# Optimization experiments

Hardware: AMD Instinct MI355X
Metric: run time of the kernel (lower is better)

## Reference

```python
import jax, jax.numpy as jnp
import numpy as np

D_MODEL = 640
KW = 32                                  # kernel_width -> content_kernel (compression (1,1))
SUPER = np.array([5, 5, 2, 1, 1])        # supersampling per subhead
DIL = np.array([1, 1, 2, 4, 8])          # dilation rate per subhead
SUBHEADS = 5
HEADS = int(SUPER.sum())                 # 14
DH = D_MODEL // SUBHEADS                 # 128
B, N = 2, 1024
KC = KW                                  # content kernel width
DIL_PER_HEAD = np.repeat(DIL, SUPER)     # dilation used by each of the 14 value heads


def _windows(seq, bias, dil):
    """Banded (dilated, stride-1, 'same'-padded) windows of a projected sequence.

    seq: (B, N, DH). The original zero-pads the raw sequence, then applies the
    per-head Linear; projecting a zero vector yields the bias, so padding the
    projected sequence with `bias` is mathematically identical.
    Returns (B, N, KC, DH) with out[b, l, j] = padded[b, l + j*dil].
    """
    dil = int(dil)
    pad_total = (KC - 1) * dil           # effective kernel minus 1, stride 1 -> same length
    pl = pad_total // 2
    pr = pad_total - pl
    b = seq.shape[0]
    left = jnp.broadcast_to(bias, (b, pl, DH))
    right = jnp.broadcast_to(bias, (b, pr, DH))
    padded = jnp.concatenate([left, seq, right], axis=1)
    idx = jnp.arange(N)[:, None] + jnp.arange(KC)[None, :] * dil  # (N, KC)
    return padded[:, idx]


def setup_inputs() -> dict:
    key = jax.random.key(0)
    ks = jax.random.split(key, 13)
    f = lambda k, sh, s=1.0: jax.random.normal(k, sh, dtype=jnp.float32) * s
    return {
        "query": f(ks[0], (B, N, D_MODEL)),
        "key": f(ks[1], (B, N, D_MODEL)),
        "value": f(ks[2], (B, N, D_MODEL)),
        "Qk": f(ks[3], (SUBHEADS, DH, D_MODEL), 0.04),
        "Qb": f(ks[4], (SUBHEADS, DH), 0.02),
        "Kk": f(ks[5], (SUBHEADS, DH, D_MODEL), 0.04),
        "Kb": f(ks[6], (SUBHEADS, DH), 0.02),
        "Vk": f(ks[7], (HEADS, DH, D_MODEL), 0.04),
        "Vb": f(ks[8], (HEADS, DH), 0.02),
        "Sk": f(ks[9], (HEADS, KC, KC), 0.1),   # Pos_Sampling kernel, Kq=1 so in=out=KC
        "Sb": f(ks[10], (HEADS, KC), 0.02),
        "Ck": f(ks[11], (D_MODEL, HEADS * DH), 0.02),  # Collapse kernel
        "Cb": f(ks[12], (D_MODEL,), 0.0),
    }


def reference(query, key, value, Qk, Qb, Kk, Kb, Vk, Vb, Sk, Sb, Ck, Cb):
    # Per-subhead Q/K projections (query_kernel=1, stride=1 -> one query per position)
    q = jnp.einsum('bnd,sod->bnso', query, Qk) + Qb          # (B,N,5,DH)
    kproj = jnp.einsum('bnd,sod->bnso', key, Kk) + Kb        # (B,N,5,DH)
    kwin = jnp.stack(
        [_windows(kproj[:, :, s], Kb[s], DIL[s]) for s in range(SUBHEADS)],
        axis=2)                                              # (B,N,5,KC,DH)
    # Banded scores (original applies no 1/sqrt(d) scaling)
    score = jnp.einsum('bnsd,bnskd->bnsk', q, kwin)          # (B,N,5,KC)
    # Supersample subhead scores into heads, then learned positional resampling
    score = jnp.repeat(score, SUPER, axis=2, total_repeat_length=HEADS)  # (B,N,14,KC)
    score = jnp.einsum('bnhk,hjk->bnhj', score, Sk) + Sb     # Pos_Sampling Linear
    w = jax.nn.softmax(score, axis=-1)
    # Per-head value projection; each head windows with its subhead's dilation
    vproj = jnp.einsum('bnd,hod->bnho', value, Vk) + Vb      # (B,N,14,DH)
    vwin = jnp.stack(
        [_windows(vproj[:, :, h], Vb[h], DIL_PER_HEAD[h]) for h in range(HEADS)],
        axis=2)                                              # (B,N,14,KC,DH)
    attn = jnp.einsum('bnhk,bnhkd->bnhd', w, vwin)           # (B,N,14,DH)
    flat = attn.reshape(attn.shape[0], attn.shape[1], HEADS * DH)
    return jnp.einsum('bnf,of->bno', flat, Ck) + Cb          # (B,N,D_MODEL)
```

## Files before the change

kernel.cpp:

```cpp
#include <hip/hip_runtime.h>
#include <hip/hip_bf16.h>

using bf16 = __hip_bfloat16;
typedef __attribute__((ext_vector_type(8))) short s16x8;
typedef __attribute__((ext_vector_type(4))) float f32x4;
typedef unsigned int u32;

__device__ __forceinline__ float b2f(short u) {
    union { float f; u32 i; } x; x.i = ((u32)(unsigned short)u) << 16; return x.f;
}
__device__ __forceinline__ short f2b(float f) {
    bf16 h = (bf16)f; return *(short*)&h;
}

__device__ __forceinline__ void glds16(const bf16* g, bf16* l) {
#if __has_builtin(__builtin_amdgcn_global_load_lds)
    __builtin_amdgcn_global_load_lds(
        (const __attribute__((address_space(1))) u32*)g,
        (__attribute__((address_space(3))) u32*)l, 16, 0, 0);
#else
    *(uint4*)l = *(const uint4*)g;
#endif
}

__global__ void sniff_kernel(const u32* __restrict__ probe, int* __restrict__ flag) {
    __shared__ int bad;
    if (threadIdx.x == 0) bad = 0;
    __syncthreads();
    int myb = 0;
    for (int i = threadIdx.x; i < 512; i += 256) {
        u32 e = (probe[i] >> 7) & 0xFFu;
        if (e >= 0xF0u) myb = 1;
    }
    if (myb) atomicOr(&bad, 1);
    __syncthreads();
    if (threadIdx.x == 0) *flag = bad ? 1 : 0;
}

struct CvtArgs {
    const void* src[13];
    bf16* dst[13];
    int n[13];
    int bb[14];
};
__global__ __launch_bounds__(256)
void convert_kernel(CvtArgs a, const int* __restrict__ flagp) {
    const int f32 = *flagp;
    const int blk = blockIdx.x;
    int s = 0;
    while (s < 12 && blk >= a.bb[s + 1]) ++s;
    const int base = (blk - a.bb[s]) * 1024 + threadIdx.x * 4;
    if (base >= a.n[s]) return;
    bf16* dst = a.dst[s] + base;
    if (f32) {
        float4 v = *((const float4*)a.src[s] + (base >> 2));
        dst[0] = (bf16)v.x; dst[1] = (bf16)v.y; dst[2] = (bf16)v.z; dst[3] = (bf16)v.w;
    } else {
        *(ushort4*)dst = *((const ushort4*)a.src[s] + (base >> 2));
    }
}

template<int BM, int BN, int OUT>
__global__ __launch_bounds__(256)
void gemm_v2(const bf16* __restrict__ A0, const bf16* __restrict__ W0,
             const bf16* __restrict__ b0, void* __restrict__ o0,
             const bf16* __restrict__ A1, const bf16* __restrict__ W1,
             const bf16* __restrict__ b1, void* __restrict__ o1,
             int M, int N, int K, const int* __restrict__ flagp) {
    const bf16* A    = blockIdx.z ? A1 : A0;
    const bf16* W    = blockIdx.z ? W1 : W0;
    const bf16* bias = blockIdx.z ? b1 : b0;
    void*       out  = blockIdx.z ? o1 : o0;
    constexpr int WM = BM / 2, WN = BN / 2, FM = WM / 16, FN = WN / 16;
    constexpr int SA = (BM * 4) / 256, SB = (BN * 4) / 256;
    __shared__ __align__(16) bf16 lA[BM * 32];
    __shared__ __align__(16) bf16 lB[BN * 32];
    const int tid = threadIdx.x;
    const int wave = tid >> 6, lane = tid & 63;
    const int wr = wave >> 1, wc = wave & 1;
    const int quad = lane >> 4, lm = lane & 15;
    const int m0 = blockIdx.x * BM, n0 = blockIdx.y * BN;
    f32x4 acc[FM][FN] = {};
    for (int k0 = 0; k0 < K; k0 += 32) {
#pragma unroll
        for (int q = 0; q < SA; ++q) {
            int sl = q * 256 + tid;
            glds16(A + (size_t)(m0 + (sl >> 2)) * K + k0 + (sl & 3) * 8, lA + sl * 8);
        }
#pragma unroll
        for (int q = 0; q < SB; ++q) {
            int sl = q * 256 + tid;
            glds16(W + (size_t)(n0 + (sl >> 2)) * K + k0 + (sl & 3) * 8, lB + sl * 8);
        }
        __syncthreads();
        s16x8 afr[FM], bfr[FN];
#pragma unroll
        for (int i = 0; i < FM; ++i)
            afr[i] = *(const s16x8*)&lA[(wr * WM + i * 16 + lm) * 32 + quad * 8];
#pragma unroll
        for (int j = 0; j < FN; ++j)
            bfr[j] = *(const s16x8*)&lB[(wc * WN + j * 16 + lm) * 32 + quad * 8];
#pragma unroll
        for (int i = 0; i < FM; ++i)
#pragma unroll
            for (int j = 0; j < FN; ++j)
                acc[i][j] = __builtin_amdgcn_mfma_f32_16x16x32_bf16(afr[i], bfr[j], acc[i][j], 0, 0, 0);
        __syncthreads();
    }
    const int f32out = (OUT == 0) ? 1 : (OUT == 1) ? 0 : *flagp;
#pragma unroll
    for (int i = 0; i < FM; ++i) {
        const int rbase = m0 + wr * WM + i * 16 + quad * 4;
#pragma unroll
        for (int j = 0; j < FN; ++j) {
            const int col = n0 + wc * WN + j * 16 + lm;
            const float bv = (float)bias[col];
#pragma unroll
            for (int r = 0; r < 4; ++r) {
                float v = acc[i][j][r] + bv;
                size_t off = (size_t)(rbase + r) * N + col;
                if (f32out) ((float*)out)[off] = v;
                else        ((bf16*)out)[off] = (bf16)v;
            }
        }
    }
}

__global__ __launch_bounds__(256)
void attn_v2(const float* __restrict__ qp, const float* __restrict__ kp,
             const bf16* __restrict__ vp,
             const bf16* __restrict__ Kbc, const bf16* __restrict__ Vbc,
             const bf16* __restrict__ Skc, const bf16* __restrict__ Sbc,
             bf16* __restrict__ atn) {
    const int pos = blockIdx.x, b = pos >> 10, l = pos & 1023;
    const int t = threadIdx.x;
    __shared__ float qs[640];
    __shared__ float partA[5 * 256];
    __shared__ float sc5[5 * 32];
    __shared__ float sc14[14 * 32];
    __shared__ float w14[14 * 32];

    for (int i = t; i < 640; i += 256) qs[i] = qp[(size_t)pos * 640 + i];
    __syncthreads();

    {
        const int j = t >> 3, part = t & 7, cbase = part * 16;
#pragma unroll
        for (int s = 0; s < 5; ++s) {
            const int dil = (s < 2) ? 1 : (1 << (s - 1));
            const int pl = (31 * dil) >> 1;
            const int row = l + j * dil - pl;
            const float* q = qs + s * 128 + cbase;
            float acc = 0.f;
            if (row >= 0 && row < 1024) {
                const float* kr = kp + (size_t)((b << 10) | row) * 640 + s * 128 + cbase;
#pragma unroll
                for (int c = 0; c < 16; c += 4) {
                    float4 kv = *(const float4*)(kr + c);
                    acc += q[c] * kv.x + q[c + 1] * kv.y + q[c + 2] * kv.z + q[c + 3] * kv.w;
                }
            } else {
                const bf16* kb = Kbc + s * 128 + cbase;
#pragma unroll
                for (int c = 0; c < 16; ++c) acc += q[c] * (float)kb[c];
            }
            partA[s * 256 + t] = acc;
        }
    }
    __syncthreads();
    if (t < 160) {
        const int s = t >> 5, j = t & 31;
        const float* p = partA + s * 256 + j * 8;
        sc5[s * 32 + j] = ((p[0] + p[1]) + (p[2] + p[3])) + ((p[4] + p[5]) + (p[6] + p[7]));
    }
    __syncthreads();

    {
        int idx = t;
#pragma unroll
        for (int rep = 0; rep < 2; ++rep, idx += 256) {
            if (idx < 448) {
                const int h = idx >> 5;
                const int s = (h < 5) ? 0 : (h < 10) ? 1 : (h < 12) ? 2 : (h == 12) ? 3 : 4;
                float acc = b2f(((const short*)Sbc)[idx]);
                const short* sk = (const short*)Skc + idx * 32;
                const float* sc = sc5 + s * 32;
#pragma unroll
                for (int k = 0; k < 32; ++k) acc += sc[k] * b2f(sk[k]);
                sc14[idx] = acc;
            }
        }
    }
    __syncthreads();

    if (t < 14) {
        const float* srow = sc14 + t * 32;
        float* wrow = w14 + t * 32;
        float mx = srow[0];
        for (int j = 1; j < 32; ++j) mx = fmaxf(mx, srow[j]);
        float sum = 0.f;
        for (int j = 0; j < 32; ++j) { float e = __expf(srow[j] - mx); wrow[j] = e; sum += e; }
        float inv = 1.f / sum;
        for (int j = 0; j < 32; ++j) wrow[j] *= inv;
    }
    __syncthreads();

    if (t < 224) {
        const int h = t >> 4, d8 = (t & 15) * 8;
        const int dil = (h < 10) ? 1 : (h < 12) ? 2 : (h == 12) ? 4 : 8;
        const int pl = (31 * dil) >> 1;
        const int col = h * 128 + d8;
        const float* wrow = w14 + h * 32;
        float acc[8] = {};
#pragma unroll
        for (int j = 0; j < 32; ++j) {
            const int row = l + j * dil - pl;
            const short* src = (row >= 0 && row < 1024)
                ? (const short*)vp + (size_t)((b << 10) | row) * 1792 + col
                : (const short*)Vbc + col;
            s16x8 v8 = *(const s16x8*)src;
            const float w = wrow[j];
#pragma unroll
            for (int r = 0; r < 8; ++r) acc[r] += w * b2f(v8[r]);
        }
        union { uint4 u; short h16[8]; } o;
#pragma unroll
        for (int r = 0; r < 8; ++r) o.h16[r] = f2b(acc[r]);
        *(uint4*)((short*)atn + (size_t)pos * 1792 + col) = o.u;
    }
}

extern "C" void kernel_launch(void* const* d_in, const int* in_sizes, int n_in,
                              void* d_out, int out_size, void* d_ws, size_t ws_size,
                              hipStream_t stream) {
    const int M = 2048;
    char* w = (char*)d_ws;
    size_t off = 0;
    auto alloc = [&](size_t bytes) -> char* {
        off = (off + 255) & ~(size_t)255;
        char* p = w + off; off += bytes; return p;
    };
    int*  flagp = (int*)alloc(4);
    bf16* qc  = (bf16*)alloc((size_t)M * 640 * 2);
    bf16* kc  = (bf16*)alloc((size_t)M * 640 * 2);
    bf16* vc  = (bf16*)alloc((size_t)M * 640 * 2);
    bf16* Qkc = (bf16*)alloc(409600 * 2);
    bf16* Kkc = (bf16*)alloc(409600 * 2);
    bf16* Vkc = (bf16*)alloc(1146880 * 2);
    bf16* Ckc = (bf16*)alloc(1146880 * 2);
    bf16* Qbc = (bf16*)alloc(640 * 2);
    bf16* Kbc = (bf16*)alloc(640 * 2);
    bf16* Vbc = (bf16*)alloc(1792 * 2);
    bf16* Skc = (bf16*)alloc(14336 * 2);
    bf16* Sbc = (bf16*)alloc(448 * 2);
    bf16* Cbc = (bf16*)alloc(640 * 2);
    float* qp = (float*)alloc((size_t)M * 640 * 4);
    float* kp = (float*)alloc((size_t)M * 640 * 4);
    bf16*  vp = (bf16*)alloc((size_t)M * 1792 * 2);
    bf16*  atn = qc;

    dim3 blk(256);
    sniff_kernel<<<dim3(1), blk, 0, stream>>>((const u32*)d_in[3], flagp);

    CvtArgs ca;
    const int srcIdx[13] = {0, 1, 2, 3, 4, 5, 6, 7, 8, 9, 10, 11, 12};
    bf16* dsts[13] = {qc, kc, vc, Qkc, Qbc, Kkc, Kbc, Vkc, Vbc, Skc, Sbc, Ckc, Cbc};
    const int ns[13] = {1310720, 1310720, 1310720, 409600, 640, 409600, 640,
                        1146880, 1792, 14336, 448, 1146880, 640};
    int cum = 0;
    for (int i = 0; i < 13; ++i) {
        ca.src[i] = d_in[srcIdx[i]];
        ca.dst[i] = dsts[i];
        ca.n[i] = ns[i];
        ca.bb[i] = cum;
        cum += (ns[i] + 1023) / 1024;
    }
    ca.bb[13] = cum;
    convert_kernel<<<dim3(cum), blk, 0, stream>>>(ca, flagp);

    gemm_v2<64, 64, 0><<<dim3(32, 10, 2), blk, 0, stream>>>(
        qc, Qkc, Qbc, qp, kc, Kkc, Kbc, kp, M, 640, 640, flagp);
    gemm_v2<64, 64, 1><<<dim3(32, 28, 1), blk, 0, stream>>>(
        vc, Vkc, Vbc, vp, vc, Vkc, Vbc, vp, M, 1792, 640, flagp);
    attn_v2<<<dim3(2048), blk, 0, stream>>>(qp, kp, vp, Kbc, Vbc, Skc, Sbc, atn);
    gemm_v2<64, 64, 2><<<dim3(32, 10, 1), blk, 0, stream>>>(
        atn, Ckc, Cbc, d_out, atn, Ckc, Cbc, d_out, M, 640, 1792, flagp);
}
```

Measured before the change: 183.1 us.

## Fuse QKV projections into one kernel and drop the dtype sniff and activation conversion

Removes the dtype-sniff kernel and the runtime flag, assuming fp32 inputs. The activations are no longer converted to bf16 in a separate pass; the projection GEMM reads fp32 directly and converts while staging into LDS. The Q, K and V projections are merged into one launch, and block indices are remapped in the GEMM and attention kernels to group work by XCD for L2 locality. This cuts launches and a full read/write of the activations. The cost is that the A tile is now loaded synchronously instead of through the global-to-LDS load path.

```diff
diff --git a/kernel.cpp b/kernel.cpp
--- a/kernel.cpp
+++ b/kernel.cpp
@@ -23,116 +23,119 @@
 #endif
 }
 
-__global__ void sniff_kernel(const u32* __restrict__ probe, int* __restrict__ flag) {
-    __shared__ int bad;
-    if (threadIdx.x == 0) bad = 0;
-    __syncthreads();
-    int myb = 0;
-    for (int i = threadIdx.x; i < 512; i += 256) {
-        u32 e = (probe[i] >> 7) & 0xFFu;
-        if (e >= 0xF0u) myb = 1;
-    }
-    if (myb) atomicOr(&bad, 1);
-    __syncthreads();
-    if (threadIdx.x == 0) *flag = bad ? 1 : 0;
-}
-
-struct CvtArgs {
-    const void* src[13];
-    bf16* dst[13];
-    int n[13];
-    int bb[14];
-};
-__global__ __launch_bounds__(256)
-void convert_kernel(CvtArgs a, const int* __restrict__ flagp) {
-    const int f32 = *flagp;
+struct CvtArgs { const float* src[10]; bf16* dst[10]; int n[10]; int bb[11]; };
+__global__ __launch_bounds__(256)
+void convert_kernel(CvtArgs a) {
     const int blk = blockIdx.x;
     int s = 0;
-    while (s < 12 && blk >= a.bb[s + 1]) ++s;
+    while (s < 9 && blk >= a.bb[s + 1]) ++s;
     const int base = (blk - a.bb[s]) * 1024 + threadIdx.x * 4;
     if (base >= a.n[s]) return;
-    bf16* dst = a.dst[s] + base;
-    if (f32) {
-        float4 v = *((const float4*)a.src[s] + (base >> 2));
-        dst[0] = (bf16)v.x; dst[1] = (bf16)v.y; dst[2] = (bf16)v.z; dst[3] = (bf16)v.w;
-    } else {
-        *(ushort4*)dst = *((const ushort4*)a.src[s] + (base >> 2));
-    }
-}
-
-template<int BM, int BN, int OUT>
-__global__ __launch_bounds__(256)
-void gemm_v2(const bf16* __restrict__ A0, const bf16* __restrict__ W0,
-             const bf16* __restrict__ b0, void* __restrict__ o0,
-             const bf16* __restrict__ A1, const bf16* __restrict__ W1,
-             const bf16* __restrict__ b1, void* __restrict__ o1,
-             int M, int N, int K, const int* __restrict__ flagp) {
-    const bf16* A    = blockIdx.z ? A1 : A0;
-    const bf16* W    = blockIdx.z ? W1 : W0;
-    const bf16* bias = blockIdx.z ? b1 : b0;
-    void*       out  = blockIdx.z ? o1 : o0;
-    constexpr int WM = BM / 2, WN = BN / 2, FM = WM / 16, FN = WN / 16;
-    constexpr int SA = (BM * 4) / 256, SB = (BN * 4) / 256;
-    __shared__ __align__(16) bf16 lA[BM * 32];
-    __shared__ __align__(16) bf16 lB[BN * 32];
+    float4 v = *(const float4*)(a.src[s] + base);
+    ushort4 o;
+    o.x = (unsigned short)f2b(v.x); o.y = (unsigned short)f2b(v.y);
+    o.z = (unsigned short)f2b(v.z); o.w = (unsigned short)f2b(v.w);
+    *(ushort4*)(a.dst[s] + base) = o;
+}
+
+template<bool A_F32, bool OUT_F32>
+__device__ __forceinline__ void gemm64(
+    const void* __restrict__ A, const bf16* __restrict__ W,
+    const bf16* __restrict__ bias, void* __restrict__ out,
+    int m0, int n0, int N, int K, bf16* lA, bf16* lB) {
     const int tid = threadIdx.x;
     const int wave = tid >> 6, lane = tid & 63;
     const int wr = wave >> 1, wc = wave & 1;
     const int quad = lane >> 4, lm = lane & 15;
-    const int m0 = blockIdx.x * BM, n0 = blockIdx.y * BN;
-    f32x4 acc[FM][FN] = {};
+    const int srow = tid >> 2, scol8 = (tid & 3) * 8;
+    f32x4 acc[2][2] = {};
     for (int k0 = 0; k0 < K; k0 += 32) {
-#pragma unroll
-        for (int q = 0; q < SA; ++q) {
-            int sl = q * 256 + tid;
-            glds16(A + (size_t)(m0 + (sl >> 2)) * K + k0 + (sl & 3) * 8, lA + sl * 8);
-        }
-#pragma unroll
-        for (int q = 0; q < SB; ++q) {
-            int sl = q * 256 + tid;
-            glds16(W + (size_t)(n0 + (sl >> 2)) * K + k0 + (sl & 3) * 8, lB + sl * 8);
-        }
+        if (A_F32) {
+            const float* g = (const float*)A + (size_t)(m0 + srow) * K + k0 + scol8;
+            float4 f0 = *(const float4*)g;
+            float4 f1 = *(const float4*)(g + 4);
+            union { uint4 u; short h[8]; } p;
+            p.h[0] = f2b(f0.x); p.h[1] = f2b(f0.y); p.h[2] = f2b(f0.z); p.h[3] = f2b(f0.w);
+            p.h[4] = f2b(f1.x); p.h[5] = f2b(f1.y); p.h[6] = f2b(f1.z); p.h[7] = f2b(f1.w);
+            *(uint4*)(lA + tid * 8) = p.u;
+        } else {
+            glds16((const bf16*)A + (size_t)(m0 + srow) * K + k0 + scol8, lA + tid * 8);
+        }
+        glds16(W + (size_t)(n0 + srow) * K + k0 + scol8, lB + tid * 8);
         __syncthreads();
-        s16x8 afr[FM], bfr[FN];
-#pragma unroll
-        for (int i = 0; i < FM; ++i)
-            afr[i] = *(const s16x8*)&lA[(wr * WM + i * 16 + lm) * 32 + quad * 8];
-#pragma unroll
-        for (int j = 0; j < FN; ++j)
-            bfr[j] = *(const s16x8*)&lB[(wc * WN + j * 16 + lm) * 32 + quad * 8];
-#pragma unroll
-        for (int i = 0; i < FM; ++i)
-#pragma unroll
-            for (int j = 0; j < FN; ++j)
-                acc[i][j] = __builtin_amdgcn_mfma_f32_16x16x32_bf16(afr[i], bfr[j], acc[i][j], 0, 0, 0);
+        s16x8 af[2], bf[2];
+#pragma unroll
+        for (int i = 0; i < 2; ++i)
+            af[i] = *(const s16x8*)&lA[(wr * 32 + i * 16 + lm) * 32 + quad * 8];
+#pragma unroll
+        for (int j = 0; j < 2; ++j)
+            bf[j] = *(const s16x8*)&lB[(wc * 32 + j * 16 + lm) * 32 + quad * 8];
+#pragma unroll
+        for (int i = 0; i < 2; ++i)
+#pragma unroll
+            for (int j = 0; j < 2; ++j)
+                acc[i][j] = __builtin_amdgcn_mfma_f32_16x16x32_bf16(af[i], bf[j], acc[i][j], 0, 0, 0);
         __syncthreads();
     }
-    const int f32out = (OUT == 0) ? 1 : (OUT == 1) ? 0 : *flagp;
-#pragma unroll
-    for (int i = 0; i < FM; ++i) {
-        const int rbase = m0 + wr * WM + i * 16 + quad * 4;
-#pragma unroll
-        for (int j = 0; j < FN; ++j) {
-            const int col = n0 + wc * WN + j * 16 + lm;
+#pragma unroll
+    for (int i = 0; i < 2; ++i) {
+        const int rbase = m0 + wr * 32 + i * 16 + quad * 4;
+#pragma unroll
+        for (int j = 0; j < 2; ++j) {
+            const int col = n0 + wc * 32 + j * 16 + lm;
             const float bv = (float)bias[col];
 #pragma unroll
             for (int r = 0; r < 4; ++r) {
                 float v = acc[i][j][r] + bv;
                 size_t off = (size_t)(rbase + r) * N + col;
-                if (f32out) ((float*)out)[off] = v;
-                else        ((bf16*)out)[off] = (bf16)v;
+                if (OUT_F32) ((float*)out)[off] = v;
+                else         ((bf16*)out)[off] = (bf16)v;
             }
         }
     }
 }
 
 __global__ __launch_bounds__(256)
-void attn_v2(const float* __restrict__ qp, const float* __restrict__ kp,
+void proj_kernel(const float* __restrict__ q, const float* __restrict__ k,
+                 const float* __restrict__ v,
+                 const bf16* __restrict__ Qkc, const bf16* __restrict__ Kkc,
+                 const bf16* __restrict__ Vkc,
+                 const bf16* __restrict__ Qbc, const bf16* __restrict__ Kbc,
+                 const bf16* __restrict__ Vbc,
+                 float* __restrict__ qp, float* __restrict__ kp,
+                 bf16* __restrict__ vp) {
+    __shared__ __align__(16) bf16 lA[64 * 32];
+    __shared__ __align__(16) bf16 lB[64 * 32];
+    const int L = blockIdx.x, xcd = L & 7, i = L >> 3;
+    const int m0 = (xcd * 4 + i / 48) * 64;
+    const int nid = i % 48;
+    if (nid < 10)
+        gemm64<true, true >(q, Qkc, Qbc, qp, m0, nid * 64, 640, 640, lA, lB);
+    else if (nid < 20)
+        gemm64<true, true >(k, Kkc, Kbc, kp, m0, (nid - 10) * 64, 640, 640, lA, lB);
+    else
+        gemm64<true, false>(v, Vkc, Vbc, vp, m0, (nid - 20) * 64, 1792, 640, lA, lB);
+}
+
+__global__ __launch_bounds__(256)
+void collapse_kernel(const bf16* __restrict__ atn, const bf16* __restrict__ Ckc,
+                     const bf16* __restrict__ Cbc, float* __restrict__ out) {
+    __shared__ __align__(16) bf16 lA[64 * 32];
+    __shared__ __align__(16) bf16 lB[64 * 32];
+    const int L = blockIdx.x, xcd = L & 7, i = L >> 3;
+    const int m0 = (xcd * 4 + i / 10) * 64;
+    const int n0 = (i % 10) * 64;
+    gemm64<false, true>(atn, Ckc, Cbc, out, m0, n0, 640, 1792, lA, lB);
+}
+
+__global__ __launch_bounds__(256)
+void attn_v3(const float* __restrict__ qp, const float* __restrict__ kp,
              const bf16* __restrict__ vp,
              const bf16* __restrict__ Kbc, const bf16* __restrict__ Vbc,
              const bf16* __restrict__ Skc, const bf16* __restrict__ Sbc,
              bf16* __restrict__ atn) {
-    const int pos = blockIdx.x, b = pos >> 10, l = pos & 1023;
+    const int pos = ((blockIdx.x & 7) << 8) | (blockIdx.x >> 3);
+    const int b = pos >> 10, l = pos & 1023;
     const int t = threadIdx.x;
     __shared__ float qs[640];
     __shared__ float partA[5 * 256];
@@ -144,7 +147,7 @@
     __syncthreads();
 
     {
-        const int j = t >> 3, part = t & 7, cbase = part * 16;
+        const int j = t >> 3, cbase = (t & 7) * 16;
 #pragma unroll
         for (int s = 0; s < 5; ++s) {
             const int dil = (s < 2) ? 1 : (1 << (s - 1));
@@ -175,21 +178,19 @@
     }
     __syncthreads();
 
-    {
-        int idx = t;
-#pragma unroll
-        for (int rep = 0; rep < 2; ++rep, idx += 256) {
-            if (idx < 448) {
-                const int h = idx >> 5;
-                const int s = (h < 5) ? 0 : (h < 10) ? 1 : (h < 12) ? 2 : (h == 12) ? 3 : 4;
-                float acc = b2f(((const short*)Sbc)[idx]);
-                const short* sk = (const short*)Skc + idx * 32;
-                const float* sc = sc5 + s * 32;
-#pragma unroll
-                for (int k = 0; k < 32; ++k) acc += sc[k] * b2f(sk[k]);
-                sc14[idx] = acc;
-            }
-        }
+    for (int idx = t; idx < 448; idx += 256) {
+        const int h = idx >> 5;
+        const int s = (h < 5) ? 0 : (h < 10) ? 1 : (h < 12) ? 2 : (h == 12) ? 3 : 4;
+        const s16x8* sk = (const s16x8*)((const short*)Skc + idx * 32);
+        const float* sc = sc5 + s * 32;
+        float acc = b2f(((const short*)Sbc)[idx]);
+#pragma unroll
+        for (int g = 0; g < 4; ++g) {
+            s16x8 kk = sk[g];
+#pragma unroll
+            for (int r = 0; r < 8; ++r) acc += sc[g * 8 + r] * b2f(kk[r]);
+        }
+        sc14[idx] = acc;
     }
     __syncthreads();
 
@@ -240,49 +241,39 @@
         off = (off + 255) & ~(size_t)255;
         char* p = w + off; off += bytes; return p;
     };
-    int*  flagp = (int*)alloc(4);
-    bf16* qc  = (bf16*)alloc((size_t)M * 640 * 2);
-    bf16* kc  = (bf16*)alloc((size_t)M * 640 * 2);
-    bf16* vc  = (bf16*)alloc((size_t)M * 640 * 2);
     bf16* Qkc = (bf16*)alloc(409600 * 2);
+    bf16* Qbc = (bf16*)alloc(640 * 2);
     bf16* Kkc = (bf16*)alloc(409600 * 2);
+    bf16* Kbc = (bf16*)alloc(640 * 2);
     bf16* Vkc = (bf16*)alloc(1146880 * 2);
-    bf16* Ckc = (bf16*)alloc(1146880 * 2);
-    bf16* Qbc = (bf16*)alloc(640 * 2);
-    bf16* Kbc = (bf16*)alloc(640 * 2);
     bf16* Vbc = (bf16*)alloc(1792 * 2);
     bf16* Skc = (bf16*)alloc(14336 * 2);
     bf16* Sbc = (bf16*)alloc(448 * 2);
+    bf16* Ckc = (bf16*)alloc(1146880 * 2);
     bf16* Cbc = (bf16*)alloc(640 * 2);
     float* qp = (float*)alloc((size_t)M * 640 * 4);
     float* kp = (float*)alloc((size_t)M * 640 * 4);
     bf16*  vp = (bf16*)alloc((size_t)M * 1792 * 2);
-    bf16*  atn = qc;
-
-    dim3 blk(256);
-    sniff_kernel<<<dim3(1), blk, 0, stream>>>((const u32*)d_in[3], flagp);
+    bf16*  atn = (bf16*)alloc((size_t)M * 1792 * 2);
 
     CvtArgs ca;
-    const int srcIdx[13] = {0, 1, 2, 3, 4, 5, 6, 7, 8, 9, 10, 11, 12};
-    bf16* dsts[13] = {qc, kc, vc, Qkc, Qbc, Kkc, Kbc, Vkc, Vbc, Skc, Sbc, Ckc, Cbc};
-    const int ns[13] = {1310720, 1310720, 1310720, 409600, 640, 409600, 640,
-                        1146880, 1792, 14336, 448, 1146880, 640};
+    bf16* dsts[10] = {Qkc, Qbc, Kkc, Kbc, Vkc, Vbc, Skc, Sbc, Ckc, Cbc};
+    const int ns[10] = {409600, 640, 409600, 640, 1146880, 1792, 14336, 448, 1146880, 640};
     int cum = 0;
-    for (int i = 0; i < 13; ++i) {
-        ca.src[i] = d_in[srcIdx[i]];
+    for (int i = 0; i < 10; ++i) {
+        ca.src[i] = (const float*)d_in[3 + i];
         ca.dst[i] = dsts[i];
         ca.n[i] = ns[i];
         ca.bb[i] = cum;
         cum += (ns[i] + 1023) / 1024;
     }
-    ca.bb[13] = cum;
-    convert_kernel<<<dim3(cum), blk, 0, stream>>>(ca, flagp);
-
-    gemm_v2<64, 64, 0><<<dim3(32, 10, 2), blk, 0, stream>>>(
-        qc, Qkc, Qbc, qp, kc, Kkc, Kbc, kp, M, 640, 640, flagp);
-    gemm_v2<64, 64, 1><<<dim3(32, 28, 1), blk, 0, stream>>>(
-        vc, Vkc, Vbc, vp, vc, Vkc, Vbc, vp, M, 1792, 640, flagp);
-    attn_v2<<<dim3(2048), blk, 0, stream>>>(qp, kp, vp, Kbc, Vbc, Skc, Sbc, atn);
-    gemm_v2<64, 64, 2><<<dim3(32, 10, 1), blk, 0, stream>>>(
-        atn, Ckc, Cbc, d_out, atn, Ckc, Cbc, d_out, M, 640, 1792, flagp);
-}
+    ca.bb[10] = cum;
+
+    dim3 blk(256);
+    convert_kernel<<<dim3(cum), blk, 0, stream>>>(ca);
+    proj_kernel<<<dim3(32 * 48), blk, 0, stream>>>(
+        (const float*)d_in[0], (const float*)d_in[1], (const float*)d_in[2],
+        Qkc, Kkc, Vkc, Qbc, Kbc, Vbc, qp, kp, vp);
+    attn_v3<<<dim3(2048), blk, 0, stream>>>(qp, kp, vp, Kbc, Vbc, Skc, Sbc, atn);
+    collapse_kernel<<<dim3(320), blk, 0, stream>>>(atn, Ckc, Cbc, (float*)d_out);
+}
```

Result: no change. 183.1 us (-0.0%).
